# Optimization experiments

Measured on AMD Instinct MI355X. Metric: run time of the kernel, lower is better.

## Reference

```python
import jax, jax.numpy as jnp
import numpy as np

B, T, E, S = 16, 2048, 1024, 2000
HID = 150
GI = 3 * E


def _mlp(x, W1, b1, W2, b2, W3, b3):
    # Score module: Linear->ReLU->(Dropout eval=id)->Linear->ReLU->(Dropout)->Linear(->1)
    h = jax.nn.relu(x @ W1 + b1)
    h = jax.nn.relu(h @ W2 + b2)
    return h @ W3 + b3


def setup_inputs() -> dict:
    key = jax.random.key(0)
    ks = jax.random.split(key, 16)
    batch_embeds = jax.random.normal(ks[0], (B, T, E), dtype=jnp.float32)
    starts = jnp.sort(jax.random.randint(ks[1], (B, S), 0, T - 33), axis=-1)
    lengths = jax.random.randint(ks[2], (B, S), 0, 24)
    num_spans = jax.random.randint(ks[3], (B,), 1, S + 1)
    sc = 0.02
    p = lambda k, shape: jax.random.normal(k, shape, dtype=jnp.float32) * sc
    return {
        "batch_embeds": batch_embeds,
        "starts": starts,
        "lengths": lengths,
        "num_spans": num_spans,
        "Wa1": p(ks[4], (E, HID)), "ba1": jnp.zeros((HID,), jnp.float32),
        "Wa2": p(ks[5], (HID, HID)), "ba2": jnp.zeros((HID,), jnp.float32),
        "Wa3": p(ks[6], (HID, 1)), "ba3": jnp.zeros((1,), jnp.float32),
        "Ws1": p(ks[7], (GI, HID)), "bs1": jnp.zeros((HID,), jnp.float32),
        "Ws2": p(ks[8], (HID, HID)), "bs2": jnp.zeros((HID,), jnp.float32),
        "Ws3": p(ks[9], (HID, 1)), "bs3": jnp.zeros((1,), jnp.float32),
    }


def reference(batch_embeds, starts, lengths, num_spans,
              Wa1, ba1, Wa2, ba2, Wa3, ba3,
              Ws1, bs1, Ws2, bs2, Ws3, bs3):
    # attention score per token: [B,T,1]
    attns = _mlp(batch_embeds, Wa1, ba1, Wa2, ba2, Wa3, ba3)
    weighted = batch_embeds * attns  # [B,T,E]
    # prefix sums turn the ragged per-span sum into two gathers per span
    csum = jnp.cumsum(weighted, axis=1)
    csum = jnp.concatenate([jnp.zeros_like(csum[:, :1]), csum], axis=1)  # [B,T+1,E]
    ends = starts + lengths  # inclusive end index, < T
    g_start = jnp.take_along_axis(batch_embeds, starts[..., None], axis=1)  # [B,S,E]
    g_end = jnp.take_along_axis(batch_embeds, ends[..., None], axis=1)      # [B,S,E]
    span_sum = (jnp.take_along_axis(csum, (ends + 1)[..., None], axis=1)
                - jnp.take_along_axis(csum, starts[..., None], axis=1))     # [B,S,E]
    span_emb = jnp.concatenate([g_start, g_end, span_sum], axis=-1)  # [B,S,3E]
    # zero-pad spans beyond each document's span count (matches torch zeros padding)
    mask = (jnp.arange(span_emb.shape[1])[None, :] < num_spans[:, None])[..., None]
    span_emb = jnp.where(mask, span_emb, jnp.zeros((), span_emb.dtype))
    mention_scores = _mlp(span_emb, Ws1, bs1, Ws2, bs2, Ws3, bs3)  # [B,S,1]
    return span_emb, mention_scores
```

## Files before the change

### kernel.cpp

```cpp
#include <hip/hip_runtime.h>
#include <hip/hip_bf16.h>

#define B_   16
#define T_   2048
#define E_   1024
#define S_   2000
#define HID_ 150
#define GI_  3072

typedef __attribute__((ext_vector_type(8))) short short8;
typedef __attribute__((ext_vector_type(4))) float f32x4;

constexpr int NPAD  = 160;
constexpr int LSTR  = 168;
constexpr int MROWS = 64;

__device__ __forceinline__ void gload16(const void* gsrc, void* ldst) {
    __builtin_amdgcn_global_load_lds(
        (const __attribute__((address_space(1))) unsigned int*)gsrc,
        (__attribute__((address_space(3))) unsigned int*)ldst,
        16, 0, 0);
}

__device__ __forceinline__ short8 pack8(float4 a, float4 b) {
    union { __hip_bfloat162 h[4]; short8 s; } u;
    u.h[0] = __float22bfloat162_rn(make_float2(a.x, a.y));
    u.h[1] = __float22bfloat162_rn(make_float2(a.z, a.w));
    u.h[2] = __float22bfloat162_rn(make_float2(b.x, b.y));
    u.h[3] = __float22bfloat162_rn(make_float2(b.z, b.w));
    return u.s;
}

__device__ __forceinline__ void store_bf16x4(__hip_bfloat16* p, float4 v) {
    union { __hip_bfloat162 h[2]; uint2 u; } cv;
    cv.h[0] = __float22bfloat162_rn(make_float2(v.x, v.y));
    cv.h[1] = __float22bfloat162_rn(make_float2(v.z, v.w));
    *reinterpret_cast<uint2*>(p) = cv.u;
}

__global__ __launch_bounds__(256)
void transpose_all(const float* __restrict__ Wa1, const float* __restrict__ Wa2,
                   const float* __restrict__ Ws1, const float* __restrict__ Ws2,
                   __hip_bfloat16* __restrict__ Wt1a, __hip_bfloat16* __restrict__ Wt2a,
                   __hip_bfloat16* __restrict__ Wt1s, __hip_bfloat16* __restrict__ Wt2s)
{
    const int s0 = 160 * 1024, s1 = 160 * 160, s2 = 160 * 3072, s3 = 160 * 160;
    int i = blockIdx.x * 256 + threadIdx.x;
    if (i < s0) {
        int n = i >> 10, k = i & 1023;
        Wt1a[i] = __float2bfloat16(n < HID_ ? Wa1[k * HID_ + n] : 0.f);
    } else if (i < s0 + s1) {
        int j = i - s0, n = j / 160, k = j - n * 160;
        Wt2a[j] = __float2bfloat16((n < HID_ && k < HID_) ? Wa2[k * HID_ + n] : 0.f);
    } else if (i < s0 + s1 + s2) {
        int j = i - s0 - s1, n = j / 3072, k = j - n * 3072;
        Wt1s[j] = __float2bfloat16(n < HID_ ? Ws1[k * HID_ + n] : 0.f);
    } else if (i < s0 + s1 + s2 + s3) {
        int j = i - s0 - s1 - s2, n = j / 160, k = j - n * 160;
        Wt2s[j] = __float2bfloat16((n < HID_ && k < HID_) ? Ws2[k * HID_ + n] : 0.f);
    }
}

template<int K1, bool BF16A>
__global__ __launch_bounds__(256, 2)
void mlp_mfma(const void* __restrict__ xin_,
              const __hip_bfloat16* __restrict__ Wt1, const float* __restrict__ b1,
              const __hip_bfloat16* __restrict__ Wt2, const float* __restrict__ b2,
              const float* __restrict__ W3, const float* __restrict__ b3,
              float* __restrict__ outp)
{
    constexpr int NC  = K1 / 64;
    constexpr int ACH = 64 * 64 * (BF16A ? 2 : 4);
    constexpr int BCH = 160 * 64 * 2;
    __shared__ __align__(16) char smem[2 * ACH + 2 * BCH];

    const int tid  = threadIdx.x;
    const int lane = tid & 63;
    const int w    = tid >> 6;
    const int rg   = w >> 1;
    const int cg   = w & 1;
    const int lr   = lane & 15;
    const int hi   = lane >> 4;

    const long long row0 = (long long)blockIdx.x * MROWS;

    auto stageA = [&](int bi, int c) {
        char* dst = smem + bi * ACH;
        if constexpr (BF16A) {
            const __hip_bfloat16* xb = (const __hip_bfloat16*)xin_;
#pragma unroll
            for (int j = 0; j < 2; ++j) {
                const int row  = (w * 2 + j) * 8 + (lane >> 3);
                const int slot = (lane & 7) ^ (row & 7);
                gload16(xb + (row0 + row) * (long long)K1 + c * 64 + slot * 8,
                        dst + (w * 2 + j) * 1024);
            }
        } else {
            const float* xf = (const float*)xin_;
#pragma unroll
            for (int j = 0; j < 4; ++j) {
                const int row  = (w * 4 + j) * 4 + (lane >> 4);
                const int slot = (lane & 15) ^ (row & 7);
                gload16(xf + (row0 + row) * (long long)K1 + c * 64 + slot * 4,
                        dst + (w * 4 + j) * 1024);
            }
        }
    };
    auto stageB = [&](int bi, int c) {
        char* dst = smem + 2 * ACH + bi * BCH;
#pragma unroll
        for (int j = 0; j < 5; ++j) {
            const int nrow = (w * 5 + j) * 8 + (lane >> 3);
            const int slot = (lane & 7) ^ (nrow & 7);
            gload16(Wt1 + (long long)nrow * K1 + c * 64 + slot * 8,
                    dst + (w * 5 + j) * 1024);
        }
    };

    f32x4 acc[2][5];
#pragma unroll
    for (int rt = 0; rt < 2; ++rt)
#pragma unroll
        for (int nt = 0; nt < 5; ++nt) acc[rt][nt] = (f32x4){0.f, 0.f, 0.f, 0.f};

    stageA(0, 0);
    stageB(0, 0);

    for (int c = 0; c < NC; ++c) {
        __syncthreads();
        if (c + 1 < NC) {
            stageA((c + 1) & 1, c + 1);
            stageB((c + 1) & 1, c + 1);
        }
        const int bi = c & 1;
        const char* sA = smem + bi * ACH;
        const char* sB = smem + 2 * ACH + bi * BCH;
#pragma unroll
        for (int ks = 0; ks < 2; ++ks) {
            short8 bfr[5];
#pragma unroll
            for (int nt = 0; nt < 5; ++nt) {
                const int nrow = cg * 80 + nt * 16 + lr;
                const int slot = (ks * 4 + hi) ^ (nrow & 7);
                bfr[nt] = *(const short8*)(sB + nrow * 128 + slot * 16);
            }
#pragma unroll
            for (int rt = 0; rt < 2; ++rt) {
                const int r = rg * 32 + rt * 16 + lr;
                short8 afr;
                if constexpr (BF16A) {
                    const int slot = (ks * 4 + hi) ^ (r & 7);
                    afr = *(const short8*)(sA + r * 128 + slot * 16);
                } else {
                    const int s0i = (ks * 8 + hi * 2) ^ (r & 7);
                    const int s1i = (ks * 8 + hi * 2 + 1) ^ (r & 7);
                    float4 a0 = *(const float4*)(sA + r * 256 + s0i * 16);
                    float4 a1 = *(const float4*)(sA + r * 256 + s1i * 16);
                    afr = pack8(a0, a1);
                }
#pragma unroll
                for (int nt = 0; nt < 5; ++nt)
                    acc[rt][nt] = __builtin_amdgcn_mfma_f32_16x16x32_bf16(
                        afr, bfr[nt], acc[rt][nt], 0, 0, 0);
            }
        }
    }
    __syncthreads();

    __hip_bfloat16* hl = (__hip_bfloat16*)smem;

#pragma unroll
    for (int nt = 0; nt < 5; ++nt) {
        const int ch = cg * 80 + nt * 16 + lr;
        const float bb = (ch < HID_) ? b1[ch] : 0.f;
#pragma unroll
        for (int rt = 0; rt < 2; ++rt)
#pragma unroll
            for (int r4 = 0; r4 < 4; ++r4) {
                const int row = rg * 32 + rt * 16 + hi * 4 + r4;
                float h = acc[rt][nt][r4] + bb;
                hl[row * LSTR + ch] = __float2bfloat16(h > 0.f ? h : 0.f);
            }
    }
    __syncthreads();

    f32x4 acc2[2][5];
#pragma unroll
    for (int rt = 0; rt < 2; ++rt)
#pragma unroll
        for (int nt = 0; nt < 5; ++nt) acc2[rt][nt] = (f32x4){0.f, 0.f, 0.f, 0.f};

#pragma unroll
    for (int ks = 0; ks < 5; ++ks) {
        const int k0 = ks * 32 + hi * 8;
        short8 bfr[5];
#pragma unroll
        for (int nt = 0; nt < 5; ++nt)
            bfr[nt] = *(const short8*)(Wt2 + (cg * 80 + nt * 16 + lr) * NPAD + k0);
#pragma unroll
        for (int rt = 0; rt < 2; ++rt) {
            short8 afr = *(const short8*)&hl[(rg * 32 + rt * 16 + lr) * LSTR + k0];
#pragma unroll
            for (int nt = 0; nt < 5; ++nt)
                acc2[rt][nt] = __builtin_amdgcn_mfma_f32_16x16x32_bf16(
                    afr, bfr[nt], acc2[rt][nt], 0, 0, 0);
        }
    }
    __syncthreads();

#pragma unroll
    for (int nt = 0; nt < 5; ++nt) {
        const int ch = cg * 80 + nt * 16 + lr;
        const float bb = (ch < HID_) ? b2[ch] : 0.f;
#pragma unroll
        for (int rt = 0; rt < 2; ++rt)
#pragma unroll
            for (int r4 = 0; r4 < 4; ++r4) {
                const int row = rg * 32 + rt * 16 + hi * 4 + r4;
                float h = acc2[rt][nt][r4] + bb;
                hl[row * LSTR + ch] = __float2bfloat16(h > 0.f ? h : 0.f);
            }
    }
    __syncthreads();

    {
        const int row = tid >> 2, quad = tid & 3;
        const int kb = quad * 38;
        const int ke = (kb + 38 > HID_) ? HID_ : kb + 38;
        float s = 0.f;
        for (int k = kb; k < ke; ++k)
            s += __bfloat162float(hl[row * LSTR + k]) * W3[k];
        s += __shfl_xor(s, 1);
        s += __shfl_xor(s, 2);
        if (quad == 0) outp[row0 + row] = s + b3[0];
    }
}

__global__ __launch_bounds__(256)
void span_kernel(const float* __restrict__ x, const float* __restrict__ attn,
                 const int* __restrict__ starts, const int* __restrict__ lengths,
                 const int* __restrict__ nspans, float* __restrict__ out,
                 __hip_bfloat16* __restrict__ shadow)
{
    const int blk = blockIdx.x;
    const int b = blk / S_;
    const int s = blk - b * S_;
    const int tid = threadIdx.x;
    float* orow = out + (long long)blk * (3 * E_);
    __hip_bfloat16* srow = shadow + (long long)blk * (3 * E_);

    if (s >= nspans[b]) {
        float4 z = make_float4(0.f, 0.f, 0.f, 0.f);
        *(float4*)(orow + tid * 4)          = z;
        *(float4*)(orow + E_ + tid * 4)     = z;
        *(float4*)(orow + 2 * E_ + tid * 4) = z;
        uint2 z2 = make_uint2(0u, 0u);
        *(uint2*)(srow + tid * 4)          = z2;
        *(uint2*)(srow + E_ + tid * 4)     = z2;
        *(uint2*)(srow + 2 * E_ + tid * 4) = z2;
        return;
    }
    const int st = starts[blk];
    const int en = st + lengths[blk];
    const float* xb = x + (long long)b * T_ * E_;

    float4 vs = *(const float4*)(xb + (long long)st * E_ + tid * 4);
    float4 ve = *(const float4*)(xb + (long long)en * E_ + tid * 4);
    *(float4*)(orow + tid * 4)      = vs;
    *(float4*)(orow + E_ + tid * 4) = ve;
    store_bf16x4(srow + tid * 4, vs);
    store_bf16x4(srow + E_ + tid * 4, ve);

    float4 a0 = make_float4(0.f, 0.f, 0.f, 0.f);
    float4 a1 = make_float4(0.f, 0.f, 0.f, 0.f);
    const float* ab = attn + b * T_;
    int t = st;
    for (; t + 1 <= en; t += 2) {
        float w0 = ab[t], w1 = ab[t + 1];
        float4 v0 = *(const float4*)(xb + (long long)t * E_ + tid * 4);
        float4 v1 = *(const float4*)(xb + (long long)(t + 1) * E_ + tid * 4);
        a0.x += v0.x * w0; a0.y += v0.y * w0; a0.z += v0.z * w0; a0.w += v0.w * w0;
        a1.x += v1.x * w1; a1.y += v1.y * w1; a1.z += v1.z * w1; a1.w += v1.w * w1;
    }
    if (t <= en) {
        float w0 = ab[t];
        float4 v0 = *(const float4*)(xb + (long long)t * E_ + tid * 4);
        a0.x += v0.x * w0; a0.y += v0.y * w0; a0.z += v0.z * w0; a0.w += v0.w * w0;
    }
    float4 a4 = make_float4(a0.x + a1.x, a0.y + a1.y, a0.z + a1.z, a0.w + a1.w);
    *(float4*)(orow + 2 * E_ + tid * 4) = a4;
    store_bf16x4(srow + 2 * E_ + tid * 4, a4);
}

extern "C" void kernel_launch(void* const* d_in, const int* in_sizes, int n_in,
                              void* d_out, int out_size, void* d_ws, size_t ws_size,
                              hipStream_t stream) {
    const float* x       = (const float*)d_in[0];
    const int*   starts  = (const int*)d_in[1];
    const int*   lengths = (const int*)d_in[2];
    const int*   nspans  = (const int*)d_in[3];
    const float* Wa1 = (const float*)d_in[4];
    const float* ba1 = (const float*)d_in[5];
    const float* Wa2 = (const float*)d_in[6];
    const float* ba2 = (const float*)d_in[7];
    const float* Wa3 = (const float*)d_in[8];
    const float* ba3 = (const float*)d_in[9];
    const float* Ws1 = (const float*)d_in[10];
    const float* bs1 = (const float*)d_in[11];
    const float* Ws2 = (const float*)d_in[12];
    const float* bs2 = (const float*)d_in[13];
    const float* Ws3 = (const float*)d_in[14];
    const float* bs3 = (const float*)d_in[15];

    float* out        = (float*)d_out;
    float* out_scores = out + (long long)B_ * S_ * 3 * E_;

    char* ws = (char*)d_ws;
    float*          attn   = (float*)ws;
    __hip_bfloat16* Wt1a   = (__hip_bfloat16*)(ws + 131072);
    __hip_bfloat16* Wt2a   = (__hip_bfloat16*)(ws + 458752);
    __hip_bfloat16* Wt1s   = (__hip_bfloat16*)(ws + 509952);
    __hip_bfloat16* Wt2s   = (__hip_bfloat16*)(ws + 1492992);
    __hip_bfloat16* shadow = (__hip_bfloat16*)(ws + 1544192);

    transpose_all<<<2760, 256, 0, stream>>>(Wa1, Wa2, Ws1, Ws2,
                                            Wt1a, Wt2a, Wt1s, Wt2s);

    mlp_mfma<E_, false><<<(B_ * T_) / MROWS, 256, 0, stream>>>
        (x, Wt1a, ba1, Wt2a, ba2, Wa3, ba3, attn);

    span_kernel<<<B_ * S_, 256, 0, stream>>>(x, attn, starts, lengths, nspans,
                                             out, shadow);

    mlp_mfma<GI_, true><<<(B_ * S_) / MROWS, 256, 0, stream>>>
        (shadow, Wt1s, bs1, Wt2s, bs2, Ws3, bs3, out_scores);
}
```

Baseline: 307.8 us.

## Fuse span embedding construction into span-score MLP, dropping bf16 shadow buffer

Replaces the separate span gather kernel and the second MLP launch with one fused kernel. Each 512-thread block builds 64 span rows chunk by chunk, writing the fp32 output and packing bf16 A tiles straight into LDS while the MFMA layer-1 GEMM consumes them. This removes the global bf16 shadow write and reread and one launch. Block IDs are remapped across XCDs. The cost is only 500 blocks with serial per-chunk span-sum loops inside the GEMM pipeline, which may limit latency hiding and parallelism.

```diff
diff --git a/kernel.cpp b/kernel.cpp
--- a/kernel.cpp
+++ b/kernel.cpp
@@ -29,13 +29,6 @@
     u.h[2] = __float22bfloat162_rn(make_float2(b.x, b.y));
     u.h[3] = __float22bfloat162_rn(make_float2(b.z, b.w));
     return u.s;
-}
-
-__device__ __forceinline__ void store_bf16x4(__hip_bfloat16* p, float4 v) {
-    union { __hip_bfloat162 h[2]; uint2 u; } cv;
-    cv.h[0] = __float22bfloat162_rn(make_float2(v.x, v.y));
-    cv.h[1] = __float22bfloat162_rn(make_float2(v.z, v.w));
-    *reinterpret_cast<uint2*>(p) = cv.u;
 }
 
 __global__ __launch_bounds__(256)
@@ -61,16 +54,16 @@
     }
 }
 
-template<int K1, bool BF16A>
+template<int K1>
 __global__ __launch_bounds__(256, 2)
-void mlp_mfma(const void* __restrict__ xin_,
+void mlp_mfma(const float* __restrict__ xin,
               const __hip_bfloat16* __restrict__ Wt1, const float* __restrict__ b1,
               const __hip_bfloat16* __restrict__ Wt2, const float* __restrict__ b2,
               const float* __restrict__ W3, const float* __restrict__ b3,
               float* __restrict__ outp)
 {
     constexpr int NC  = K1 / 64;
-    constexpr int ACH = 64 * 64 * (BF16A ? 2 : 4);
+    constexpr int ACH = 64 * 64 * 4;
     constexpr int BCH = 160 * 64 * 2;
     __shared__ __align__(16) char smem[2 * ACH + 2 * BCH];
 
@@ -86,24 +79,12 @@
 
     auto stageA = [&](int bi, int c) {
         char* dst = smem + bi * ACH;
-        if constexpr (BF16A) {
-            const __hip_bfloat16* xb = (const __hip_bfloat16*)xin_;
-#pragma unroll
-            for (int j = 0; j < 2; ++j) {
-                const int row  = (w * 2 + j) * 8 + (lane >> 3);
-                const int slot = (lane & 7) ^ (row & 7);
-                gload16(xb + (row0 + row) * (long long)K1 + c * 64 + slot * 8,
-                        dst + (w * 2 + j) * 1024);
-            }
-        } else {
-            const float* xf = (const float*)xin_;
-#pragma unroll
-            for (int j = 0; j < 4; ++j) {
-                const int row  = (w * 4 + j) * 4 + (lane >> 4);
-                const int slot = (lane & 15) ^ (row & 7);
-                gload16(xf + (row0 + row) * (long long)K1 + c * 64 + slot * 4,
-                        dst + (w * 4 + j) * 1024);
-            }
+#pragma unroll
+        for (int j = 0; j < 4; ++j) {
+            const int row  = (w * 4 + j) * 4 + (lane >> 4);
+            const int slot = (lane & 15) ^ (row & 7);
+            gload16(xin + (row0 + row) * (long long)K1 + c * 64 + slot * 4,
+                    dst + (w * 4 + j) * 1024);
         }
     };
     auto stageB = [&](int bi, int c) {
@@ -128,10 +109,7 @@
 
     for (int c = 0; c < NC; ++c) {
         __syncthreads();
-        if (c + 1 < NC) {
-            stageA((c + 1) & 1, c + 1);
-            stageB((c + 1) & 1, c + 1);
-        }
+        if (c + 1 < NC) { stageA((c + 1) & 1, c + 1); stageB((c + 1) & 1, c + 1); }
         const int bi = c & 1;
         const char* sA = smem + bi * ACH;
         const char* sB = smem + 2 * ACH + bi * BCH;
@@ -147,17 +125,11 @@
 #pragma unroll
             for (int rt = 0; rt < 2; ++rt) {
                 const int r = rg * 32 + rt * 16 + lr;
-                short8 afr;
-                if constexpr (BF16A) {
-                    const int slot = (ks * 4 + hi) ^ (r & 7);
-                    afr = *(const short8*)(sA + r * 128 + slot * 16);
-                } else {
-                    const int s0i = (ks * 8 + hi * 2) ^ (r & 7);
-                    const int s1i = (ks * 8 + hi * 2 + 1) ^ (r & 7);
-                    float4 a0 = *(const float4*)(sA + r * 256 + s0i * 16);
-                    float4 a1 = *(const float4*)(sA + r * 256 + s1i * 16);
-                    afr = pack8(a0, a1);
-                }
+                const int s0i = (ks * 8 + hi * 2) ^ (r & 7);
+                const int s1i = (ks * 8 + hi * 2 + 1) ^ (r & 7);
+                float4 a0 = *(const float4*)(sA + r * 256 + s0i * 16);
+                float4 a1 = *(const float4*)(sA + r * 256 + s1i * 16);
+                short8 afr = pack8(a0, a1);
 #pragma unroll
                 for (int nt = 0; nt < 5; ++nt)
                     acc[rt][nt] = __builtin_amdgcn_mfma_f32_16x16x32_bf16(
@@ -236,60 +208,208 @@
     }
 }
 
-__global__ __launch_bounds__(256)
-void span_kernel(const float* __restrict__ x, const float* __restrict__ attn,
-                 const int* __restrict__ starts, const int* __restrict__ lengths,
-                 const int* __restrict__ nspans, float* __restrict__ out,
-                 __hip_bfloat16* __restrict__ shadow)
+__global__ __launch_bounds__(512, 4)
+void span_score(const float* __restrict__ x, const float* __restrict__ attn,
+                const int* __restrict__ starts, const int* __restrict__ lengths,
+                const int* __restrict__ nspans,
+                const __hip_bfloat16* __restrict__ Wt1, const float* __restrict__ b1,
+                const __hip_bfloat16* __restrict__ Wt2, const float* __restrict__ b2,
+                const float* __restrict__ W3, const float* __restrict__ b3,
+                float* __restrict__ spanout, float* __restrict__ scoreout)
 {
-    const int blk = blockIdx.x;
-    const int b = blk / S_;
-    const int s = blk - b * S_;
-    const int tid = threadIdx.x;
-    float* orow = out + (long long)blk * (3 * E_);
-    __hip_bfloat16* srow = shadow + (long long)blk * (3 * E_);
-
-    if (s >= nspans[b]) {
-        float4 z = make_float4(0.f, 0.f, 0.f, 0.f);
-        *(float4*)(orow + tid * 4)          = z;
-        *(float4*)(orow + E_ + tid * 4)     = z;
-        *(float4*)(orow + 2 * E_ + tid * 4) = z;
-        uint2 z2 = make_uint2(0u, 0u);
-        *(uint2*)(srow + tid * 4)          = z2;
-        *(uint2*)(srow + E_ + tid * 4)     = z2;
-        *(uint2*)(srow + 2 * E_ + tid * 4) = z2;
-        return;
-    }
-    const int st = starts[blk];
-    const int en = st + lengths[blk];
-    const float* xb = x + (long long)b * T_ * E_;
-
-    float4 vs = *(const float4*)(xb + (long long)st * E_ + tid * 4);
-    float4 ve = *(const float4*)(xb + (long long)en * E_ + tid * 4);
-    *(float4*)(orow + tid * 4)      = vs;
-    *(float4*)(orow + E_ + tid * 4) = ve;
-    store_bf16x4(srow + tid * 4, vs);
-    store_bf16x4(srow + E_ + tid * 4, ve);
-
-    float4 a0 = make_float4(0.f, 0.f, 0.f, 0.f);
-    float4 a1 = make_float4(0.f, 0.f, 0.f, 0.f);
-    const float* ab = attn + b * T_;
-    int t = st;
-    for (; t + 1 <= en; t += 2) {
-        float w0 = ab[t], w1 = ab[t + 1];
-        float4 v0 = *(const float4*)(xb + (long long)t * E_ + tid * 4);
-        float4 v1 = *(const float4*)(xb + (long long)(t + 1) * E_ + tid * 4);
-        a0.x += v0.x * w0; a0.y += v0.y * w0; a0.z += v0.z * w0; a0.w += v0.w * w0;
-        a1.x += v1.x * w1; a1.y += v1.y * w1; a1.z += v1.z * w1; a1.w += v1.w * w1;
-    }
-    if (t <= en) {
-        float w0 = ab[t];
-        float4 v0 = *(const float4*)(xb + (long long)t * E_ + tid * 4);
-        a0.x += v0.x * w0; a0.y += v0.y * w0; a0.z += v0.z * w0; a0.w += v0.w * w0;
-    }
-    float4 a4 = make_float4(a0.x + a1.x, a0.y + a1.y, a0.z + a1.z, a0.w + a1.w);
-    *(float4*)(orow + 2 * E_ + tid * 4) = a4;
-    store_bf16x4(srow + 2 * E_ + tid * 4, a4);
+    __shared__ __align__(16) char smem[58112];
+    int* stL = (int*)(smem + 57344);
+    int* enL = (int*)(smem + 57600);
+    int* bL  = (int*)(smem + 57856);
+
+    const int tid  = threadIdx.x;
+    const int lane = tid & 63;
+    const int w    = tid >> 6;
+    const int rg   = w >> 1;
+    const int cg   = w & 1;
+    const int lr   = lane & 15;
+    const int hi   = lane >> 4;
+
+    int bid = blockIdx.x;
+    {
+        const int qq = 500 / 8, rr = 500 % 8;
+        const int xcd = bid % 8, i = bid / 8;
+        bid = (xcd < rr ? xcd * (qq + 1) : rr * (qq + 1) + (xcd - rr) * qq) + i;
+    }
+    const int span0 = bid * 64;
+
+    if (tid < 64) {
+        const int sp = span0 + tid;
+        const int b  = sp / S_;
+        const int s  = sp - b * S_;
+        const bool val = s < nspans[b];
+        const int st = val ? starts[sp] : 0;
+        stL[tid] = st;
+        enL[tid] = val ? (st + lengths[sp]) : -1;
+        bL[tid]  = b;
+    }
+    __syncthreads();
+
+    const int r    = tid >> 3;
+    const int q    = tid & 7;
+    const int st_r = stL[r];
+    const int en_r = enL[r];
+    const long long sp_r = span0 + r;
+    const float* xb = x + (long long)bL[r] * T_ * E_;
+    const float* ab = attn + bL[r] * T_;
+
+    auto constructA = [&](int bi, int c) {
+        float4 v0, v1;
+        if (c < 32) {
+            if (en_r >= st_r) {
+                const int srow = (c < 16) ? st_r : en_r;
+                const float* p = xb + (long long)srow * E_ + (c & 15) * 64 + q * 8;
+                v0 = *(const float4*)p;
+                v1 = *(const float4*)(p + 4);
+            } else {
+                v0 = make_float4(0.f, 0.f, 0.f, 0.f);
+                v1 = make_float4(0.f, 0.f, 0.f, 0.f);
+            }
+        } else {
+            const int cl = (c - 32) * 64 + q * 8;
+            float4 s0 = make_float4(0.f,0.f,0.f,0.f), s1 = s0, s2 = s0, s3 = s0;
+            int t = st_r;
+            for (; t + 1 <= en_r; t += 2) {
+                const float a0 = ab[t], a1 = ab[t + 1];
+                const float* p0 = xb + (long long)t * E_ + cl;
+                const float4 u0 = *(const float4*)p0;
+                const float4 u1 = *(const float4*)(p0 + 4);
+                const float4 z0 = *(const float4*)(p0 + E_);
+                const float4 z1 = *(const float4*)(p0 + E_ + 4);
+                s0.x += u0.x*a0; s0.y += u0.y*a0; s0.z += u0.z*a0; s0.w += u0.w*a0;
+                s1.x += u1.x*a0; s1.y += u1.y*a0; s1.z += u1.z*a0; s1.w += u1.w*a0;
+                s2.x += z0.x*a1; s2.y += z0.y*a1; s2.z += z0.z*a1; s2.w += z0.w*a1;
+                s3.x += z1.x*a1; s3.y += z1.y*a1; s3.z += z1.z*a1; s3.w += z1.w*a1;
+            }
+            if (t <= en_r) {
+                const float a0 = ab[t];
+                const float* p0 = xb + (long long)t * E_ + cl;
+                const float4 u0 = *(const float4*)p0;
+                const float4 u1 = *(const float4*)(p0 + 4);
+                s0.x += u0.x*a0; s0.y += u0.y*a0; s0.z += u0.z*a0; s0.w += u0.w*a0;
+                s1.x += u1.x*a0; s1.y += u1.y*a0; s1.z += u1.z*a0; s1.w += u1.w*a0;
+            }
+            v0 = make_float4(s0.x+s2.x, s0.y+s2.y, s0.z+s2.z, s0.w+s2.w);
+            v1 = make_float4(s1.x+s3.x, s1.y+s3.y, s1.z+s3.z, s1.w+s3.w);
+        }
+        float* orow = spanout + sp_r * (3 * E_) + c * 64 + q * 8;
+        *(float4*)orow       = v0;
+        *(float4*)(orow + 4) = v1;
+        *(short8*)(smem + bi * 8192 + r * 128 + ((q ^ (r & 7)) * 16)) = pack8(v0, v1);
+    };
+
+    auto stageB = [&](int bi, int c) {
+        char* dst = smem + 16384 + bi * 20480;
+#pragma unroll
+        for (int j = 0; j < 3; ++j) {
+            const int idx = w * 3 + j;
+            if (idx < 20) {
+                const int nrow = idx * 8 + (lane >> 3);
+                const int slot = (lane & 7) ^ (nrow & 7);
+                gload16(Wt1 + (long long)nrow * GI_ + c * 64 + slot * 8,
+                        dst + idx * 1024);
+            }
+        }
+    };
+
+    f32x4 acc[5];
+#pragma unroll
+    for (int nt = 0; nt < 5; ++nt) acc[nt] = (f32x4){0.f, 0.f, 0.f, 0.f};
+
+    constructA(0, 0);
+    stageB(0, 0);
+
+    for (int c = 0; c < 48; ++c) {
+        __syncthreads();
+        if (c + 1 < 48) stageB((c + 1) & 1, c + 1);
+        const int bi = c & 1;
+        const char* sAc = smem + bi * 8192;
+        const char* sBc = smem + 16384 + bi * 20480;
+#pragma unroll
+        for (int ks = 0; ks < 2; ++ks) {
+            short8 bfr[5];
+#pragma unroll
+            for (int nt = 0; nt < 5; ++nt) {
+                const int nrow = cg * 80 + nt * 16 + lr;
+                const int slot = (ks * 4 + hi) ^ (nrow & 7);
+                bfr[nt] = *(const short8*)(sBc + nrow * 128 + slot * 16);
+            }
+            const int r2 = rg * 16 + lr;
+            const int sl = (ks * 4 + hi) ^ (r2 & 7);
+            short8 afr = *(const short8*)(sAc + r2 * 128 + sl * 16);
+#pragma unroll
+            for (int nt = 0; nt < 5; ++nt)
+                acc[nt] = __builtin_amdgcn_mfma_f32_16x16x32_bf16(
+                    afr, bfr[nt], acc[nt], 0, 0, 0);
+        }
+        if (c + 1 < 48) constructA((c + 1) & 1, c + 1);
+    }
+    __syncthreads();
+
+    __hip_bfloat16* hl = (__hip_bfloat16*)smem;
+
+#pragma unroll
+    for (int nt = 0; nt < 5; ++nt) {
+        const int ch = cg * 80 + nt * 16 + lr;
+        const float bb = (ch < HID_) ? b1[ch] : 0.f;
+#pragma unroll
+        for (int r4 = 0; r4 < 4; ++r4) {
+            const int row = rg * 16 + hi * 4 + r4;
+            float h = acc[nt][r4] + bb;
+            hl[row * LSTR + ch] = __float2bfloat16(h > 0.f ? h : 0.f);
+        }
+    }
+    __syncthreads();
+
+    f32x4 acc2[5];
+#pragma unroll
+    for (int nt = 0; nt < 5; ++nt) acc2[nt] = (f32x4){0.f, 0.f, 0.f, 0.f};
+
+#pragma unroll
+    for (int ks = 0; ks < 5; ++ks) {
+        const int k0 = ks * 32 + hi * 8;
+        short8 bfr[5];
+#pragma unroll
+        for (int nt = 0; nt < 5; ++nt)
+            bfr[nt] = *(const short8*)(Wt2 + (cg * 80 + nt * 16 + lr) * NPAD + k0);
+        short8 afr = *(const short8*)&hl[(rg * 16 + lr) * LSTR + k0];
+#pragma unroll
+        for (int nt = 0; nt < 5; ++nt)
+            acc2[nt] = __builtin_amdgcn_mfma_f32_16x16x32_bf16(
+                afr, bfr[nt], acc2[nt], 0, 0, 0);
+    }
+    __syncthreads();
+
+#pragma unroll
+    for (int nt = 0; nt < 5; ++nt) {
+        const int ch = cg * 80 + nt * 16 + lr;
+        const float bb = (ch < HID_) ? b2[ch] : 0.f;
+#pragma unroll
+        for (int r4 = 0; r4 < 4; ++r4) {
+            const int row = rg * 16 + hi * 4 + r4;
+            float h = acc2[nt][r4] + bb;
+            hl[row * LSTR + ch] = __float2bfloat16(h > 0.f ? h : 0.f);
+        }
+    }
+    __syncthreads();
+
+    {
+        const int row = tid >> 3, oct = tid & 7;
+        const int kb = oct * 19;
+        const int ke = (kb + 19 > HID_) ? HID_ : kb + 19;
+        float s = 0.f;
+        for (int k = kb; k < ke; ++k)
+            s += __bfloat162float(hl[row * LSTR + k]) * W3[k];
+        s += __shfl_xor(s, 1);
+        s += __shfl_xor(s, 2);
+        s += __shfl_xor(s, 4);
+        if (oct == 0) scoreout[span0 + row] = s + b3[0];
+    }
 }
 
 extern "C" void kernel_launch(void* const* d_in, const int* in_sizes, int n_in,
@@ -316,22 +436,19 @@
     float* out_scores = out + (long long)B_ * S_ * 3 * E_;
 
     char* ws = (char*)d_ws;
-    float*          attn   = (float*)ws;
-    __hip_bfloat16* Wt1a   = (__hip_bfloat16*)(ws + 131072);
-    __hip_bfloat16* Wt2a   = (__hip_bfloat16*)(ws + 458752);
-    __hip_bfloat16* Wt1s   = (__hip_bfloat16*)(ws + 509952);
-    __hip_bfloat16* Wt2s   = (__hip_bfloat16*)(ws + 1492992);
-    __hip_bfloat16* shadow = (__hip_bfloat16*)(ws + 1544192);
+    float*          attn = (float*)ws;
+    __hip_bfloat16* Wt1a = (__hip_bfloat16*)(ws + 131072);
+    __hip_bfloat16* Wt2a = (__hip_bfloat16*)(ws + 458752);
+    __hip_bfloat16* Wt1s = (__hip_bfloat16*)(ws + 509952);
+    __hip_bfloat16* Wt2s = (__hip_bfloat16*)(ws + 1492992);
 
     transpose_all<<<2760, 256, 0, stream>>>(Wa1, Wa2, Ws1, Ws2,
                                             Wt1a, Wt2a, Wt1s, Wt2s);
 
-    mlp_mfma<E_, false><<<(B_ * T_) / MROWS, 256, 0, stream>>>
+    mlp_mfma<E_><<<(B_ * T_) / MROWS, 256, 0, stream>>>
         (x, Wt1a, ba1, Wt2a, ba2, Wa3, ba3, attn);
 
-    span_kernel<<<B_ * S_, 256, 0, stream>>>(x, attn, starts, lengths, nspans,
-                                             out, shadow);
-
-    mlp_mfma<GI_, true><<<(B_ * S_) / MROWS, 256, 0, stream>>>
-        (shadow, Wt1s, bs1, Wt2s, bs2, Ws3, bs3, out_scores);
-}
+    span_score<<<500, 512, 0, stream>>>
+        (x, attn, starts, lengths, nspans,
+         Wt1s, bs1, Wt2s, bs2, Ws3, bs3, out, out_scores);
+}
```

New measurement: 269.3 us. 12.5% less time.
